# Performance work log

Measured on AMD Instinct MI355X. Metric: run time of the kernel, lower is better.

## Reference

```python
import jax, jax.numpy as jnp
import numpy as np
import math

HIDDEN = 4096
N_HEADS = 32
N_KV_HEADS = 8
HEAD_DIM = HIDDEN // N_HEADS  # 128
ROPE_THETA = 10000.0
BATCH = 1
SEQ = 2048
NEG_INF = jnp.finfo(jnp.float32).min


def setup_inputs() -> dict:
    key = jax.random.key(0)
    ks = jax.random.split(key, 7)
    s = 0.02
    hidden_states = jax.random.normal(ks[0], (BATCH, SEQ, HIDDEN), jnp.float32)
    residual = jax.random.normal(ks[1], (BATCH, SEQ, HIDDEN), jnp.float32)
    Wq = jax.random.normal(ks[2], (HIDDEN, HIDDEN), jnp.float32) * s
    Wk = jax.random.normal(ks[3], (N_KV_HEADS * HEAD_DIM, HIDDEN), jnp.float32) * s
    Wv = jax.random.normal(ks[4], (N_KV_HEADS * HEAD_DIM, HIDDEN), jnp.float32) * s
    Wo = jax.random.normal(ks[5], (HIDDEN, HIDDEN), jnp.float32) * s
    # additive causal mask, shape (bsz, 1, q_len, kv_len)
    causal = jnp.tril(jnp.ones((SEQ, SEQ), jnp.bool_))
    attention_mask = jnp.where(causal, 0.0, NEG_INF)[None, None, :, :].astype(jnp.float32)
    position_ids = jnp.broadcast_to(jnp.arange(SEQ, dtype=jnp.int64), (BATCH, SEQ))
    return {
        "hidden_states": hidden_states, "residual": residual,
        "Wq": Wq, "Wk": Wk, "Wv": Wv, "Wo": Wo,
        "attention_mask": attention_mask, "position_ids": position_ids,
    }


def _rope_cos_sin(position_ids):
    # inv_freq: (head_dim/2,)
    inv_freq = 1.0 / (ROPE_THETA ** (jnp.arange(0, HEAD_DIM, 2, dtype=jnp.float32) / HEAD_DIM))
    # angles: (b, s, head_dim/2)
    ang = position_ids.astype(jnp.float32)[:, :, None] * inv_freq[None, None, :]
    # HF Llama concatenates freqs twice: cos/sin shape (b, s, head_dim)
    emb = jnp.concatenate([ang, ang], axis=-1)
    return jnp.cos(emb), jnp.sin(emb)


def _rotate_half(x):
    x1, x2 = jnp.split(x, 2, axis=-1)
    return jnp.concatenate([-x2, x1], axis=-1)


def _apply_rope(x, cos, sin):
    # x: (b, h, s, d); cos/sin: (b, s, d) -> broadcast over heads
    return x * cos[:, None, :, :] + _rotate_half(x) * sin[:, None, :, :]


def reference(hidden_states, residual, Wq, Wk, Wv, Wo, attention_mask, position_ids):
    b, s, _ = hidden_states.shape
    groups = N_HEADS // N_KV_HEADS
    # QKV projections (Llama has no bias)
    q = (hidden_states @ Wq.T).reshape(b, s, N_HEADS, HEAD_DIM).transpose(0, 2, 1, 3)
    k = (hidden_states @ Wk.T).reshape(b, s, N_KV_HEADS, HEAD_DIM).transpose(0, 2, 1, 3)
    v = (hidden_states @ Wv.T).reshape(b, s, N_KV_HEADS, HEAD_DIM).transpose(0, 2, 1, 3)
    cos, sin = _rope_cos_sin(position_ids)
    q = _apply_rope(q, cos, sin)
    k = _apply_rope(k, cos, sin)
    # repeat_kv: (b, kv_h, s, d) -> (b, h, s, d)
    k = jnp.repeat(k, groups, axis=1)
    v = jnp.repeat(v, groups, axis=1)
    scores = jnp.einsum('bhqd,bhkd->bhqk', q, k) / math.sqrt(HEAD_DIM)
    scores = jnp.maximum(scores + attention_mask, NEG_INF)
    probs = jax.nn.softmax(scores.astype(jnp.float32), axis=-1).astype(q.dtype)
    attn = jnp.einsum('bhqk,bhkd->bhqd', probs, v)  # (b, h, s, d)
    attn = attn.transpose(0, 2, 1, 3).reshape(b, s, HIDDEN)
    # fused LinearAdd: o_proj + residual
    out = attn @ Wo.T + residual
    return out
```

## Files before the change

kernel.cpp:

```cpp
#include <hip/hip_runtime.h>

#define SEQ 2048
#define HID 4096
#define NH 32
#define NKV 8
#define HD 128

typedef __attribute__((ext_vector_type(8))) short short8;
typedef __attribute__((ext_vector_type(4))) float f32x4;

#define CFENCE asm volatile("" ::: "memory")

static __device__ __forceinline__ unsigned short f2bf(float f) {
  union { float f; unsigned u; } v; v.f = f;
  return (unsigned short)((v.u + 0x7fffu + ((v.u >> 16) & 1u)) >> 16);
}
static __device__ __forceinline__ float bf2f(unsigned short h) {
  union { unsigned u; float f; } v; v.u = ((unsigned)h) << 16;
  return v.f;
}

__global__ void cvt_bf16(const float* __restrict__ in, unsigned short* __restrict__ out, int n4) {
  int i = blockIdx.x * blockDim.x + threadIdx.x;
  int st = gridDim.x * blockDim.x;
  for (; i < n4; i += st) {
    float4 v = reinterpret_cast<const float4*>(in)[i];
    ushort4 o;
    o.x = f2bf(v.x); o.y = f2bf(v.y); o.z = f2bf(v.z); o.w = f2bf(v.w);
    reinterpret_cast<ushort4*>(out)[i] = o;
  }
}

__global__ void rope_table(const int* __restrict__ pos, float* __restrict__ tab) {
  int t = blockIdx.x * blockDim.x + threadIdx.x;
  if (t >= SEQ * 64) return;
  int s = t >> 6, i = t & 63;
  float inv = powf(10000.0f, -(float)i / 64.0f);
  float ang = (float)pos[s] * inv;
  tab[s * 128 + i] = cosf(ang);
  tab[s * 128 + 64 + i] = sinf(ang);
}

__global__ void rope_apply(unsigned short* __restrict__ Q, unsigned short* __restrict__ K,
                           const float* __restrict__ tab) {
  int t = blockIdx.x * blockDim.x + threadIdx.x;
  const int QP = SEQ * NH * 64, KP = SEQ * NKV * 64;
  unsigned short* p;
  int s, i;
  if (t < QP) {
    s = t / (NH * 64); int r = t % (NH * 64);
    p = Q + (long)s * HID + (r >> 6) * HD; i = r & 63;
  } else if (t < QP + KP) {
    int u = t - QP;
    s = u / (NKV * 64); int r = u % (NKV * 64);
    p = K + (long)s * 1024 + (r >> 6) * HD; i = r & 63;
  } else return;
  float c = tab[s * 128 + i], sn = tab[s * 128 + 64 + i];
  float x1 = bf2f(p[i]), x2 = bf2f(p[i + 64]);
  p[i]      = f2bf(x1 * c - x2 * sn);
  p[i + 64] = f2bf(x2 * c + x1 * sn);
}

static __device__ __forceinline__ void gl16(const unsigned short* g, unsigned short* l) {
  __builtin_amdgcn_global_load_lds((const __attribute__((address_space(1))) unsigned int*)g,
                                   (__attribute__((address_space(3))) unsigned int*)l, 16, 0, 0);
}

static __device__ __forceinline__ void stage_half(const unsigned short* __restrict__ gsrc,
                                                  unsigned short* __restrict__ dst, int K, int t) {
#pragma unroll
  for (int p = 0; p < 2; p++) {
    int chunk = p * 512 + t;
    int row = chunk >> 3, j = chunk & 7;
    gl16(gsrc + (size_t)row * K + ((j ^ (row & 7)) << 3), dst + chunk * 8);
  }
}

template <int EPI>
__global__ __launch_bounds__(512, 2)
void gemm256(const unsigned short* __restrict__ A, const unsigned short* __restrict__ B,
             unsigned short* __restrict__ Qo, unsigned short* __restrict__ Ko,
             unsigned short* __restrict__ Vt, float* __restrict__ Cf,
             const float* __restrict__ Res, int K) {
  __shared__ unsigned short smem[65536];

  const int nwg = gridDim.x, fid = blockIdx.x;
  const int sid = (fid & 7) * (nwg >> 3) + (fid >> 3);
  const int bm = sid & 7, bn = sid >> 3;

  const int t = threadIdx.x, lane = t & 63, w = t >> 6, g = lane >> 4;
  const int wm = w >> 2, wn = w & 3;

  const unsigned short* Abase = A + (size_t)(bm * 256) * K;
  const unsigned short* Bbase = B + (size_t)(bn * 256) * K;

  stage_half(Abase,                  smem,         K, t);
  stage_half(Abase + (size_t)128 * K, smem + 8192,  K, t);
  stage_half(Bbase,                  smem + 16384, K, t);
  stage_half(Bbase + (size_t)128 * K, smem + 24576, K, t);
  asm volatile("s_waitcnt vmcnt(0)" ::: "memory");
  __syncthreads();

  f32x4 acc[8][4] = {};
  const int NT = K >> 6;

  for (int kt = 0; kt < NT; kt++) {
    const int buf = (kt & 1) << 15;
    const int nbuf = buf ^ 32768;
    const size_t knext = (size_t)(kt + 1) * 64;
    const bool prefetch = (kt + 1 < NT);
#pragma unroll
    for (int q = 0; q < 4; q++) {
      short8 af[4][2], bfv[2][2];
#pragma unroll
      for (int m2 = 0; m2 < 4; m2++) {
        const int rr = ((q >> 1) * 4 + m2) * 16 + (lane & 15);
        const unsigned short* pA = smem + buf + wm * 8192 + rr * 64;
#pragma unroll
        for (int ks = 0; ks < 2; ks++)
          af[m2][ks] = *reinterpret_cast<const short8*>(
              pA + ((ks * 32 + g * 8) ^ ((rr & 7) << 3)));
      }
#pragma unroll
      for (int n2 = 0; n2 < 2; n2++) {
        const int nl = wn * 64 + ((q & 1) * 2 + n2) * 16 + (lane & 15);
        const unsigned short* pB = smem + buf + 16384 + (nl >> 7) * 8192 + (nl & 127) * 64;
#pragma unroll
        for (int ks = 0; ks < 2; ks++)
          bfv[n2][ks] = *reinterpret_cast<const short8*>(
              pB + ((ks * 32 + g * 8) ^ ((nl & 7) << 3)));
      }
      if (prefetch) {
        if (q < 2) stage_half(Abase + (size_t)(q * 128) * K + knext, smem + nbuf + q * 8192, K, t);
        else       stage_half(Bbase + (size_t)((q - 2) * 128) * K + knext,
                              smem + nbuf + 16384 + (q - 2) * 8192, K, t);
      }
      __builtin_amdgcn_s_barrier();
      CFENCE;
      __builtin_amdgcn_s_setprio(1);
#pragma unroll
      for (int m2 = 0; m2 < 4; m2++)
#pragma unroll
        for (int n2 = 0; n2 < 2; n2++)
#pragma unroll
          for (int ks = 0; ks < 2; ks++)
            acc[(q >> 1) * 4 + m2][(q & 1) * 2 + n2] =
                __builtin_amdgcn_mfma_f32_16x16x32_bf16(af[m2][ks], bfv[n2][ks],
                    acc[(q >> 1) * 4 + m2][(q & 1) * 2 + n2], 0, 0, 0);
      __builtin_amdgcn_s_setprio(0);
      if (q == 3 && prefetch) asm volatile("s_waitcnt vmcnt(0)" ::: "memory");
      __builtin_amdgcn_s_barrier();
      CFENCE;
    }
  }

  const int r0 = bm * 256 + wm * 128 + g * 4;
  const int c0 = bn * 256 + wn * 64 + (lane & 15);
#pragma unroll
  for (int mi = 0; mi < 8; mi++)
#pragma unroll
    for (int ni = 0; ni < 4; ni++) {
      const int row = r0 + mi * 16;
      const int col = c0 + ni * 16;
      if (EPI == 1) {
#pragma unroll
        for (int j = 0; j < 4; j++) {
          size_t idx = (size_t)(row + j) * 4096 + col;
          Cf[idx] = acc[mi][ni][j] + Res[idx];
        }
      } else {
        if (col < 4096) {
#pragma unroll
          for (int j = 0; j < 4; j++)
            Qo[(size_t)(row + j) * 4096 + col] = f2bf(acc[mi][ni][j]);
        } else if (col < 5120) {
#pragma unroll
          for (int j = 0; j < 4; j++)
            Ko[(size_t)(row + j) * 1024 + (col - 4096)] = f2bf(acc[mi][ni][j]);
        } else {
          const int c = col - 5120;
          ushort4 pk;
          pk.x = f2bf(acc[mi][ni][0]); pk.y = f2bf(acc[mi][ni][1]);
          pk.z = f2bf(acc[mi][ni][2]); pk.w = f2bf(acc[mi][ni][3]);
          *reinterpret_cast<ushort4*>(
              Vt + ((size_t)((c >> 7) * 128 + (c & 127))) * 2048 + row) = pk;
        }
      }
    }
}

__global__ __launch_bounds__(256)
void attn(const unsigned short* __restrict__ Q, const unsigned short* __restrict__ Kg,
          const unsigned short* __restrict__ Vg, unsigned short* __restrict__ O) {
  const int h = blockIdx.x, qb = 31 - blockIdx.y, kvh = h >> 2;
  __shared__ unsigned short Kl[64 * 128];
  __shared__ unsigned short Vl[128 * 64];
  __shared__ unsigned short Pl[4][16 * 72];
  const int t = threadIdx.x, lane = t & 63, w = t >> 6, g = lane >> 4;

  short8 qf[4];
  {
    const int qrow = qb * 64 + w * 16 + (lane & 15);
    const unsigned short* qp = Q + (size_t)qrow * HID + h * HD + g * 8;
#pragma unroll
    for (int kf = 0; kf < 4; kf++) qf[kf] = *reinterpret_cast<const short8*>(qp + kf * 32);
  }

  f32x4 oacc[8] = {};
  float m_run[4], l_run[4];
#pragma unroll
  for (int j = 0; j < 4; j++) { m_run[j] = -3e38f; l_run[j] = 0.f; }

  const float SCL2E = 0.08838834764831845f * 1.4426950408889634f;
  const int ktiles = qb + 1;
  const int qrow_l = qb * 64 + w * 16 + g * 4;

  const unsigned short* kbase = Kg + kvh * HD;
  const unsigned short* vbase = Vg + (size_t)kvh * 128 * 2048;

  short8 kreg[4], vreg[4];
#define LOADKV(KT)                                                                     \
  {                                                                                    \
    _Pragma("unroll") for (int i = 0; i < 4; i++) {                                    \
      int slot = t + i * 256;                                                          \
      kreg[i] = *reinterpret_cast<const short8*>(                                      \
          kbase + (size_t)((KT) * 64 + (slot >> 4)) * 1024 + (slot & 15) * 8);         \
      vreg[i] = *reinterpret_cast<const short8*>(                                      \
          vbase + (size_t)(slot >> 3) * 2048 + (KT) * 64 + (slot & 7) * 8);            \
    }                                                                                  \
  }

  LOADKV(0);

  for (int kt = 0; kt < ktiles; kt++) {
    __syncthreads();
#pragma unroll
    for (int i = 0; i < 4; i++) {
      int slot = t + i * 256;
      int kr = slot >> 4, kc = slot & 15;
      *reinterpret_cast<short8*>(Kl + kr * 128 + ((((kc * 16) ^ ((kr & 7) << 4))) >> 1)) = kreg[i];
      int vr = slot >> 3, vc = slot & 7;
      *reinterpret_cast<short8*>(Vl + vr * 64 + ((((vc * 16) ^ ((vr & 7) << 4))) >> 1)) = vreg[i];
    }
    __syncthreads();

    if (kt + 1 < ktiles) LOADKV(kt + 1);

    f32x4 sacc[4] = {};
#pragma unroll
    for (int nt = 0; nt < 4; nt++) {
      int row = nt * 16 + (lane & 15);
#pragma unroll
      for (int kf = 0; kf < 4; kf++) {
        short8 kfr = *reinterpret_cast<const short8*>(
            Kl + row * 128 + (((kf * 64 + g * 16) ^ ((row & 7) << 4)) >> 1));
        sacc[nt] = __builtin_amdgcn_mfma_f32_16x16x32_bf16(qf[kf], kfr, sacc[nt], 0, 0, 0);
      }
    }

    float mt[4];
    if (kt == qb) {
      const int kc0 = kt * 64 + (lane & 15);
#pragma unroll
      for (int j = 0; j < 4; j++)
#pragma unroll
        for (int nt = 0; nt < 4; nt++)
          if (kc0 + nt * 16 > qrow_l + j) sacc[nt][j] = -3e38f;
    }
#pragma unroll
    for (int j = 0; j < 4; j++)
      mt[j] = fmaxf(fmaxf(sacc[0][j], sacc[1][j]), fmaxf(sacc[2][j], sacc[3][j]));
#pragma unroll
    for (int d = 1; d < 16; d <<= 1)
#pragma unroll
      for (int j = 0; j < 4; j++) mt[j] = fmaxf(mt[j], __shfl_xor(mt[j], d));

    float rs[4], prow[4];
#pragma unroll
    for (int j = 0; j < 4; j++) {
      float mn = fmaxf(m_run[j], mt[j]);
      rs[j] = exp2f((m_run[j] - mn) * SCL2E);
      m_run[j] = mn;
      float mnl = mn * SCL2E;
      float p0 = exp2f(sacc[0][j] * SCL2E - mnl);
      float p1 = exp2f(sacc[1][j] * SCL2E - mnl);
      float p2 = exp2f(sacc[2][j] * SCL2E - mnl);
      float p3 = exp2f(sacc[3][j] * SCL2E - mnl);
      sacc[0][j] = p0; sacc[1][j] = p1; sacc[2][j] = p2; sacc[3][j] = p3;
      prow[j] = (p0 + p1) + (p2 + p3);
    }
#pragma unroll
    for (int d = 1; d < 16; d <<= 1)
#pragma unroll
      for (int j = 0; j < 4; j++) prow[j] += __shfl_xor(prow[j], d);
#pragma unroll
    for (int j = 0; j < 4; j++) l_run[j] = l_run[j] * rs[j] + prow[j];
#pragma unroll
    for (int n8 = 0; n8 < 8; n8++)
#pragma unroll
      for (int j = 0; j < 4; j++) oacc[n8][j] *= rs[j];

    unsigned short* pw = &Pl[w][0];
#pragma unroll
    for (int j = 0; j < 4; j++) {
      int r = g * 4 + j;
#pragma unroll
      for (int nt = 0; nt < 4; nt++)
        pw[r * 72 + nt * 16 + (lane & 15)] = f2bf(sacc[nt][j]);
    }
    short8 pf0 = *reinterpret_cast<const short8*>(pw + (lane & 15) * 72 + g * 8);
    short8 pf1 = *reinterpret_cast<const short8*>(pw + (lane & 15) * 72 + 32 + g * 8);

#pragma unroll
    for (int n8 = 0; n8 < 8; n8++) {
      int row = n8 * 16 + (lane & 15);
      short8 vf0 = *reinterpret_cast<const short8*>(
          Vl + row * 64 + (((g * 16) ^ ((row & 7) << 4)) >> 1));
      oacc[n8] = __builtin_amdgcn_mfma_f32_16x16x32_bf16(pf0, vf0, oacc[n8], 0, 0, 0);
      short8 vf1 = *reinterpret_cast<const short8*>(
          Vl + row * 64 + (((64 + g * 16) ^ ((row & 7) << 4)) >> 1));
      oacc[n8] = __builtin_amdgcn_mfma_f32_16x16x32_bf16(pf1, vf1, oacc[n8], 0, 0, 0);
    }
  }

  float inv[4];
#pragma unroll
  for (int j = 0; j < 4; j++) inv[j] = 1.0f / l_run[j];
  const int orow = qb * 64 + w * 16 + g * 4;
#pragma unroll
  for (int n8 = 0; n8 < 8; n8++)
#pragma unroll
    for (int j = 0; j < 4; j++)
      O[(size_t)(orow + j) * HID + h * HD + n8 * 16 + (lane & 15)] = f2bf(oacc[n8][j] * inv[j]);
#undef LOADKV
}

extern "C" void kernel_launch(void* const* d_in, const int* in_sizes, int n_in,
                              void* d_out, int out_size, void* d_ws, size_t ws_size,
                              hipStream_t stream) {
  const float* hs  = (const float*)d_in[0];
  const float* res = (const float*)d_in[1];
  const float* Wq  = (const float*)d_in[2];
  const float* Wk  = (const float*)d_in[3];
  const float* Wv  = (const float*)d_in[4];
  const float* Wo  = (const float*)d_in[5];
  const int* pos   = (const int*)d_in[7];
  float* out = (float*)d_out;

  char* w = (char*)d_ws;
  unsigned short* hsb  = (unsigned short*)w; w += (size_t)SEQ * HID * 2;
  unsigned short* wqb  = (unsigned short*)w; w += (size_t)HID * HID * 2;
  unsigned short* wkvb = (unsigned short*)w; w += (size_t)2048 * HID * 2;
  unsigned short* wob  = (unsigned short*)w; w += (size_t)HID * HID * 2;
  unsigned short* Qb   = (unsigned short*)w; w += (size_t)SEQ * HID * 2;
  unsigned short* Kb   = (unsigned short*)w; w += (size_t)SEQ * 1024 * 2;
  unsigned short* Vtb  = (unsigned short*)w; w += (size_t)NKV * 128 * SEQ * 2;
  unsigned short* Ab   = (unsigned short*)w; w += (size_t)SEQ * HID * 2;
  float* tab           = (float*)w;          w += (size_t)SEQ * 128 * 4;

  cvt_bf16<<<2048, 256, 0, stream>>>(hs, hsb, SEQ * HID / 4);
  cvt_bf16<<<2048, 256, 0, stream>>>(Wq, wqb, HID * HID / 4);
  cvt_bf16<<<1024, 256, 0, stream>>>(Wk, wkvb, 1024 * HID / 4);
  cvt_bf16<<<1024, 256, 0, stream>>>(Wv, wkvb + (size_t)1024 * HID, 1024 * HID / 4);
  cvt_bf16<<<2048, 256, 0, stream>>>(Wo, wob, HID * HID / 4);
  rope_table<<<SEQ * 64 / 256, 256, 0, stream>>>(pos, tab);

  gemm256<3><<<192, 512, 0, stream>>>(hsb, wqb, Qb, Kb, Vtb, nullptr, nullptr, HID);

  rope_apply<<<(SEQ * NH * 64 + SEQ * NKV * 64) / 256, 256, 0, stream>>>(Qb, Kb, tab);

  attn<<<dim3(32, 32), 256, 0, stream>>>(Qb, Kb, Vtb, Ab);

  gemm256<1><<<128, 512, 0, stream>>>(Ab, wob, nullptr, nullptr, nullptr, out, res, HID);
}
```

Baseline: 626.0 us.

## Retile GEMMs to 128xBN with XCD-aware mapping and fuse conversion launches

Replaces the 256x256 GEMM with a templated 128xBN tile (BN=384 for QKV, 256 for o_proj). The grid becomes 256 workgroups, which fills more CUs than the previous 192 and 128, and an XCD-aware block mapping keeps L2 reuse local. The k-loop is restructured into four MFMA phases with the next tile's loads staged in between. The five fp32-to-bf16 conversion launches are merged into one kernel. The cost is lower arithmetic intensity per tile and more global traffic per FLOP.

```diff
diff --git a/kernel.cpp b/kernel.cpp
--- a/kernel.cpp
+++ b/kernel.cpp
@@ -20,14 +20,29 @@
   return v.f;
 }
 
-__global__ void cvt_bf16(const float* __restrict__ in, unsigned short* __restrict__ out, int n4) {
+__global__ void cvt_all(const float* __restrict__ hs, const float* __restrict__ wq,
+                        const float* __restrict__ wk, const float* __restrict__ wv,
+                        const float* __restrict__ wo,
+                        unsigned short* __restrict__ hsb, unsigned short* __restrict__ wqb,
+                        unsigned short* __restrict__ wkvb, unsigned short* __restrict__ wob) {
+  const int S0 = 2097152;
+  const int S1 = S0 + 4194304;
+  const int S2 = S1 + 1048576;
+  const int S3 = S2 + 1048576;
+  const int S4 = S3 + 4194304;
   int i = blockIdx.x * blockDim.x + threadIdx.x;
   int st = gridDim.x * blockDim.x;
-  for (; i < n4; i += st) {
-    float4 v = reinterpret_cast<const float4*>(in)[i];
+  for (; i < S4; i += st) {
+    const float4* src; ushort4* dst; int off;
+    if (i < S0)      { src = (const float4*)hs; dst = (ushort4*)hsb;  off = i; }
+    else if (i < S1) { src = (const float4*)wq; dst = (ushort4*)wqb;  off = i - S0; }
+    else if (i < S2) { src = (const float4*)wk; dst = (ushort4*)wkvb; off = i - S1; }
+    else if (i < S3) { src = (const float4*)wv; dst = (ushort4*)wkvb + 1048576; off = i - S2; }
+    else             { src = (const float4*)wo; dst = (ushort4*)wob;  off = i - S3; }
+    float4 v = src[off];
     ushort4 o;
     o.x = f2bf(v.x); o.y = f2bf(v.y); o.z = f2bf(v.z); o.w = f2bf(v.w);
-    reinterpret_cast<ushort4*>(out)[i] = o;
+    dst[off] = o;
   }
 }
 
@@ -66,8 +81,8 @@
                                    (__attribute__((address_space(3))) unsigned int*)l, 16, 0, 0);
 }
 
-static __device__ __forceinline__ void stage_half(const unsigned short* __restrict__ gsrc,
-                                                  unsigned short* __restrict__ dst, int K, int t) {
+static __device__ __forceinline__ void stage128(const unsigned short* __restrict__ gsrc,
+                                                unsigned short* __restrict__ dst, int K, int t) {
 #pragma unroll
   for (int p = 0; p < 2; p++) {
     int chunk = p * 512 + t;
@@ -76,112 +91,151 @@
   }
 }
 
-template <int EPI>
+template <int BN, int EPI>
 __global__ __launch_bounds__(512, 2)
-void gemm256(const unsigned short* __restrict__ A, const unsigned short* __restrict__ B,
-             unsigned short* __restrict__ Qo, unsigned short* __restrict__ Ko,
-             unsigned short* __restrict__ Vt, float* __restrict__ Cf,
-             const float* __restrict__ Res, int K) {
-  __shared__ unsigned short smem[65536];
-
-  const int nwg = gridDim.x, fid = blockIdx.x;
-  const int sid = (fid & 7) * (nwg >> 3) + (fid >> 3);
-  const int bm = sid & 7, bn = sid >> 3;
-
-  const int t = threadIdx.x, lane = t & 63, w = t >> 6, g = lane >> 4;
+void gemm8p(const unsigned short* __restrict__ A, const unsigned short* __restrict__ B,
+            unsigned short* __restrict__ Qo, unsigned short* __restrict__ Ko,
+            unsigned short* __restrict__ Vt, float* __restrict__ Cf,
+            const float* __restrict__ Res, int K) {
+  constexpr int NF   = BN / 64;
+  constexpr int NH2  = NF / 2;
+  constexpr int NBG  = BN / 128;
+  constexpr int BUFE = 8192 + BN * 64;
+  __shared__ unsigned short smem[2 * BUFE];
+
+  const int fid = blockIdx.x;
+  const int xcd = fid & 7, idx = fid >> 3;
+  const int bm = (xcd & 3) * 4 + (idx & 3);
+  const int bn = (xcd >> 2) * 8 + (idx >> 2);
+
+  const int t = threadIdx.x, lane = t & 63, w = t >> 6, g = lane >> 4, l15 = lane & 15;
   const int wm = w >> 2, wn = w & 3;
 
-  const unsigned short* Abase = A + (size_t)(bm * 256) * K;
-  const unsigned short* Bbase = B + (size_t)(bn * 256) * K;
-
-  stage_half(Abase,                  smem,         K, t);
-  stage_half(Abase + (size_t)128 * K, smem + 8192,  K, t);
-  stage_half(Bbase,                  smem + 16384, K, t);
-  stage_half(Bbase + (size_t)128 * K, smem + 24576, K, t);
+  const unsigned short* Abase = A + (size_t)(bm * 128) * K;
+  const unsigned short* Bbase = B + (size_t)(bn * BN) * K;
+
+  stage128(Abase, smem, K, t);
+#pragma unroll
+  for (int gi = 0; gi < NBG; gi++)
+    stage128(Bbase + (size_t)(gi * 128) * K, smem + 8192 + gi * 8192, K, t);
   asm volatile("s_waitcnt vmcnt(0)" ::: "memory");
   __syncthreads();
 
-  f32x4 acc[8][4] = {};
+  f32x4 acc[4][NF] = {};
   const int NT = K >> 6;
 
+  const int arow[4] = { wm * 64 + 0 * 16 + l15, wm * 64 + 1 * 16 + l15,
+                        wm * 64 + 2 * 16 + l15, wm * 64 + 3 * 16 + l15 };
+
   for (int kt = 0; kt < NT; kt++) {
-    const int buf = (kt & 1) << 15;
-    const int nbuf = buf ^ 32768;
+    const unsigned short* buf = smem + (kt & 1) * BUFE;
+    unsigned short* nbuf = smem + ((kt & 1) ^ 1) * BUFE;
     const size_t knext = (size_t)(kt + 1) * 64;
-    const bool prefetch = (kt + 1 < NT);
-#pragma unroll
-    for (int q = 0; q < 4; q++) {
-      short8 af[4][2], bfv[2][2];
-#pragma unroll
-      for (int m2 = 0; m2 < 4; m2++) {
-        const int rr = ((q >> 1) * 4 + m2) * 16 + (lane & 15);
-        const unsigned short* pA = smem + buf + wm * 8192 + rr * 64;
-#pragma unroll
-        for (int ks = 0; ks < 2; ks++)
-          af[m2][ks] = *reinterpret_cast<const short8*>(
-              pA + ((ks * 32 + g * 8) ^ ((rr & 7) << 3)));
-      }
-#pragma unroll
-      for (int n2 = 0; n2 < 2; n2++) {
-        const int nl = wn * 64 + ((q & 1) * 2 + n2) * 16 + (lane & 15);
-        const unsigned short* pB = smem + buf + 16384 + (nl >> 7) * 8192 + (nl & 127) * 64;
-#pragma unroll
-        for (int ks = 0; ks < 2; ks++)
-          bfv[n2][ks] = *reinterpret_cast<const short8*>(
-              pB + ((ks * 32 + g * 8) ^ ((nl & 7) << 3)));
-      }
-      if (prefetch) {
-        if (q < 2) stage_half(Abase + (size_t)(q * 128) * K + knext, smem + nbuf + q * 8192, K, t);
-        else       stage_half(Bbase + (size_t)((q - 2) * 128) * K + knext,
-                              smem + nbuf + 16384 + (q - 2) * 8192, K, t);
-      }
-      __builtin_amdgcn_s_barrier();
-      CFENCE;
-      __builtin_amdgcn_s_setprio(1);
-#pragma unroll
-      for (int m2 = 0; m2 < 4; m2++)
-#pragma unroll
-        for (int n2 = 0; n2 < 2; n2++)
-#pragma unroll
-          for (int ks = 0; ks < 2; ks++)
-            acc[(q >> 1) * 4 + m2][(q & 1) * 2 + n2] =
-                __builtin_amdgcn_mfma_f32_16x16x32_bf16(af[m2][ks], bfv[n2][ks],
-                    acc[(q >> 1) * 4 + m2][(q & 1) * 2 + n2], 0, 0, 0);
-      __builtin_amdgcn_s_setprio(0);
-      if (q == 3 && prefetch) asm volatile("s_waitcnt vmcnt(0)" ::: "memory");
-      __builtin_amdgcn_s_barrier();
-      CFENCE;
-    }
-  }
-
-  const int r0 = bm * 256 + wm * 128 + g * 4;
-  const int c0 = bn * 256 + wn * 64 + (lane & 15);
-#pragma unroll
-  for (int mi = 0; mi < 8; mi++)
-#pragma unroll
-    for (int ni = 0; ni < 4; ni++) {
-      const int row = r0 + mi * 16;
-      const int col = c0 + ni * 16;
+    const bool pf = (kt + 1 < NT);
+    short8 a[4], b[NH2];
+
+#pragma unroll
+    for (int mf = 0; mf < 4; mf++)
+      a[mf] = *reinterpret_cast<const short8*>(buf + arow[mf] * 64 + ((g * 8) ^ ((arow[mf] & 7) << 3)));
+#pragma unroll
+    for (int i = 0; i < NH2; i++) {
+      const int rb = wn * (BN / 4) + i * 16 + l15;
+      b[i] = *reinterpret_cast<const short8*>(buf + 8192 + rb * 64 + ((g * 8) ^ ((rb & 7) << 3)));
+    }
+    if (pf) {
+      stage128(Abase + knext, nbuf, K, t);
+      stage128(Bbase + knext, nbuf + 8192, K, t);
+    }
+    CFENCE; __builtin_amdgcn_s_barrier(); CFENCE;
+    __builtin_amdgcn_s_setprio(1);
+#pragma unroll
+    for (int mf = 0; mf < 4; mf++)
+#pragma unroll
+      for (int i = 0; i < NH2; i++)
+        acc[mf][i] = __builtin_amdgcn_mfma_f32_16x16x32_bf16(a[mf], b[i], acc[mf][i], 0, 0, 0);
+    __builtin_amdgcn_s_setprio(0);
+    CFENCE; __builtin_amdgcn_s_barrier(); CFENCE;
+
+#pragma unroll
+    for (int i = 0; i < NH2; i++) {
+      const int rb = wn * (BN / 4) + (NH2 + i) * 16 + l15;
+      b[i] = *reinterpret_cast<const short8*>(buf + 8192 + rb * 64 + ((g * 8) ^ ((rb & 7) << 3)));
+    }
+    if (pf) stage128(Bbase + (size_t)128 * K + knext, nbuf + 16384, K, t);
+    CFENCE; __builtin_amdgcn_s_barrier(); CFENCE;
+    __builtin_amdgcn_s_setprio(1);
+#pragma unroll
+    for (int mf = 0; mf < 4; mf++)
+#pragma unroll
+      for (int i = 0; i < NH2; i++)
+        acc[mf][NH2 + i] = __builtin_amdgcn_mfma_f32_16x16x32_bf16(a[mf], b[i], acc[mf][NH2 + i], 0, 0, 0);
+    __builtin_amdgcn_s_setprio(0);
+    CFENCE; __builtin_amdgcn_s_barrier(); CFENCE;
+
+#pragma unroll
+    for (int mf = 0; mf < 4; mf++)
+      a[mf] = *reinterpret_cast<const short8*>(buf + arow[mf] * 64 + ((32 + g * 8) ^ ((arow[mf] & 7) << 3)));
+#pragma unroll
+    for (int i = 0; i < NH2; i++) {
+      const int rb = wn * (BN / 4) + i * 16 + l15;
+      b[i] = *reinterpret_cast<const short8*>(buf + 8192 + rb * 64 + ((32 + g * 8) ^ ((rb & 7) << 3)));
+    }
+    if (pf && NBG == 3) stage128(Bbase + (size_t)256 * K + knext, nbuf + 24576, K, t);
+    CFENCE; __builtin_amdgcn_s_barrier(); CFENCE;
+    __builtin_amdgcn_s_setprio(1);
+#pragma unroll
+    for (int mf = 0; mf < 4; mf++)
+#pragma unroll
+      for (int i = 0; i < NH2; i++)
+        acc[mf][i] = __builtin_amdgcn_mfma_f32_16x16x32_bf16(a[mf], b[i], acc[mf][i], 0, 0, 0);
+    __builtin_amdgcn_s_setprio(0);
+    CFENCE; __builtin_amdgcn_s_barrier(); CFENCE;
+
+#pragma unroll
+    for (int i = 0; i < NH2; i++) {
+      const int rb = wn * (BN / 4) + (NH2 + i) * 16 + l15;
+      b[i] = *reinterpret_cast<const short8*>(buf + 8192 + rb * 64 + ((32 + g * 8) ^ ((rb & 7) << 3)));
+    }
+    CFENCE; __builtin_amdgcn_s_barrier(); CFENCE;
+    __builtin_amdgcn_s_setprio(1);
+#pragma unroll
+    for (int mf = 0; mf < 4; mf++)
+#pragma unroll
+      for (int i = 0; i < NH2; i++)
+        acc[mf][NH2 + i] = __builtin_amdgcn_mfma_f32_16x16x32_bf16(a[mf], b[i], acc[mf][NH2 + i], 0, 0, 0);
+    __builtin_amdgcn_s_setprio(0);
+    if (pf) asm volatile("s_waitcnt vmcnt(0)" ::: "memory");
+    CFENCE; __builtin_amdgcn_s_barrier(); CFENCE;
+  }
+
+  const int r0 = bm * 128 + wm * 64 + g * 4;
+  const int c0 = bn * BN + wn * (BN / 4) + l15;
+#pragma unroll
+  for (int mf = 0; mf < 4; mf++)
+#pragma unroll
+    for (int nf = 0; nf < NF; nf++) {
+      const int row = r0 + mf * 16;
+      const int col = c0 + nf * 16;
       if (EPI == 1) {
 #pragma unroll
         for (int j = 0; j < 4; j++) {
           size_t idx = (size_t)(row + j) * 4096 + col;
-          Cf[idx] = acc[mi][ni][j] + Res[idx];
+          Cf[idx] = acc[mf][nf][j] + Res[idx];
         }
       } else {
         if (col < 4096) {
 #pragma unroll
           for (int j = 0; j < 4; j++)
-            Qo[(size_t)(row + j) * 4096 + col] = f2bf(acc[mi][ni][j]);
+            Qo[(size_t)(row + j) * 4096 + col] = f2bf(acc[mf][nf][j]);
         } else if (col < 5120) {
 #pragma unroll
           for (int j = 0; j < 4; j++)
-            Ko[(size_t)(row + j) * 1024 + (col - 4096)] = f2bf(acc[mi][ni][j]);
+            Ko[(size_t)(row + j) * 1024 + (col - 4096)] = f2bf(acc[mf][nf][j]);
         } else {
           const int c = col - 5120;
           ushort4 pk;
-          pk.x = f2bf(acc[mi][ni][0]); pk.y = f2bf(acc[mi][ni][1]);
-          pk.z = f2bf(acc[mi][ni][2]); pk.w = f2bf(acc[mi][ni][3]);
+          pk.x = f2bf(acc[mf][nf][0]); pk.y = f2bf(acc[mf][nf][1]);
+          pk.z = f2bf(acc[mf][nf][2]); pk.w = f2bf(acc[mf][nf][3]);
           *reinterpret_cast<ushort4*>(
               Vt + ((size_t)((c >> 7) * 128 + (c & 127))) * 2048 + row) = pk;
         }
@@ -358,18 +412,14 @@
   unsigned short* Ab   = (unsigned short*)w; w += (size_t)SEQ * HID * 2;
   float* tab           = (float*)w;          w += (size_t)SEQ * 128 * 4;
 
-  cvt_bf16<<<2048, 256, 0, stream>>>(hs, hsb, SEQ * HID / 4);
-  cvt_bf16<<<2048, 256, 0, stream>>>(Wq, wqb, HID * HID / 4);
-  cvt_bf16<<<1024, 256, 0, stream>>>(Wk, wkvb, 1024 * HID / 4);
-  cvt_bf16<<<1024, 256, 0, stream>>>(Wv, wkvb + (size_t)1024 * HID, 1024 * HID / 4);
-  cvt_bf16<<<2048, 256, 0, stream>>>(Wo, wob, HID * HID / 4);
+  cvt_all<<<2048, 256, 0, stream>>>(hs, Wq, Wk, Wv, Wo, hsb, wqb, wkvb, wob);
   rope_table<<<SEQ * 64 / 256, 256, 0, stream>>>(pos, tab);
 
-  gemm256<3><<<192, 512, 0, stream>>>(hsb, wqb, Qb, Kb, Vtb, nullptr, nullptr, HID);
+  gemm8p<384, 3><<<256, 512, 0, stream>>>(hsb, wqb, Qb, Kb, Vtb, nullptr, nullptr, HID);
 
   rope_apply<<<(SEQ * NH * 64 + SEQ * NKV * 64) / 256, 256, 0, stream>>>(Qb, Kb, tab);
 
   attn<<<dim3(32, 32), 256, 0, stream>>>(Qb, Kb, Vtb, Ab);
 
-  gemm256<1><<<128, 512, 0, stream>>>(Ab, wob, nullptr, nullptr, nullptr, out, res, HID);
-}
+  gemm8p<256, 1><<<256, 512, 0, stream>>>(Ab, wob, nullptr, nullptr, nullptr, out, res, HID);
+}
```

Result: faster. 520.7 us (-16.8%).
